# Performance work log

Hardware: AMD Instinct MI355X
Metric: run time of the kernel (lower is better)

Reference implementation:

```python
import jax, jax.numpy as jnp
import numpy as np
import math

# Fixed representative draw of the host-side RNG (all aug probs fired).
MIRROR_X, MIRROR_Y = -1.0, 1.0      # x flip on, y flip off
TX, TY = 0.06, -0.04                # translate percents
SX, SY = 1.1, 0.95                  # anisotropic scale
ZOOM = 0.9                          # isotropic zoom (draws from params['scale'] range in source)
ROT = math.radians(27.0)            # rotate degrees -> rad
SHX, SHY = 0.05, -0.03              # shear percents


def _affine_grid(theta, H, W):
    # torch F.affine_grid with align_corners=False: pixel-center normalized coords
    xs = (jnp.arange(W, dtype=jnp.float32) + 0.5) * (2.0 / W) - 1.0
    ys = (jnp.arange(H, dtype=jnp.float32) + 0.5) * (2.0 / H) - 1.0
    gx, gy = jnp.meshgrid(xs, ys)  # [H,W]
    coords = jnp.stack([gx, gy, jnp.ones_like(gx)], axis=-1)  # [H,W,3]
    return jnp.einsum('ij,hwj->hwi', theta, coords)  # [H,W,2] (x,y); same grid for all batch


def _gather(img, iy, ix, valid):
    # img [B,C,H,W]; iy/ix [H,W] int32; valid [H,W] bool. zeros padding.
    B, C, H, W = img.shape
    idx = (jnp.clip(iy, 0, H - 1) * W + jnp.clip(ix, 0, W - 1)).reshape(-1)
    g = img.reshape(B, C, H * W)[:, :, idx].reshape(B, C, H, W)
    return jnp.where(valid[None, None], g, jnp.zeros((), img.dtype))


def _unnormalize(grid, H, W):
    # align_corners=False unnormalization
    ix = ((grid[..., 0] + 1.0) * W - 1.0) * 0.5
    iy = ((grid[..., 1] + 1.0) * H - 1.0) * 0.5
    return ix, iy


def _grid_sample_bilinear(img, grid):
    B, C, H, W = img.shape
    ix, iy = _unnormalize(grid, H, W)
    x0 = jnp.floor(ix); y0 = jnp.floor(iy)
    wx1 = ix - x0; wx0 = 1.0 - wx1
    wy1 = iy - y0; wy0 = 1.0 - wy1
    x0i = x0.astype(jnp.int32); y0i = y0.astype(jnp.int32)
    x1i = x0i + 1; y1i = y0i + 1
    inb = lambda x, y: (x >= 0) & (x < W) & (y >= 0) & (y < H)
    v00 = _gather(img, y0i, x0i, inb(x0i, y0i))
    v01 = _gather(img, y0i, x1i, inb(x1i, y0i))
    v10 = _gather(img, y1i, x0i, inb(x0i, y1i))
    v11 = _gather(img, y1i, x1i, inb(x1i, y1i))
    out = (v00 * (wy0 * wx0)[None, None] + v01 * (wy0 * wx1)[None, None]
           + v10 * (wy1 * wx0)[None, None] + v11 * (wy1 * wx1)[None, None])
    return out


def _grid_sample_nearest(img, grid):
    B, C, H, W = img.shape
    ix, iy = _unnormalize(grid, H, W)
    xi = jnp.round(ix).astype(jnp.int32)
    yi = jnp.round(iy).astype(jnp.int32)
    valid = (xi >= 0) & (xi < W) & (yi >= 0) & (yi < H)
    return _gather(img, yi, xi, valid)


def _thetas():
    c, s = math.cos(ROT), math.sin(ROT)
    return [
        jnp.array([[MIRROR_X, 0.0, 0.0], [0.0, MIRROR_Y, 0.0]], jnp.float32),  # mirror
        jnp.array([[1.0, 0.0, TX], [0.0, 1.0, TY]], jnp.float32),              # translate
        jnp.array([[SX, 0.0, 0.0], [0.0, SY, 0.0]], jnp.float32),              # scale
        jnp.array([[ZOOM, 0.0, 0.0], [0.0, ZOOM, 0.0]], jnp.float32),          # zoom
        jnp.array([[c, -s, 0.0], [s, c, 0.0]], jnp.float32),                   # rotate
        jnp.array([[1.0, SHX, 0.0], [SHY, 1.0, 0.0]], jnp.float32),            # shear
    ]


def setup_inputs() -> dict:
    key = jax.random.key(0)
    k1, k2 = jax.random.split(key)
    img = jax.random.normal(k1, (16, 3, 512, 512), dtype=jnp.float32)
    label = jax.random.uniform(k2, (16, 3, 512, 512), dtype=jnp.float32)
    return {"img": img, "label": label}


def reference(img, label):
    B, C, H, W = img.shape
    # Sequential resampling, exactly as the torch module: one affine_grid +
    # grid_sample pair per enabled augmentation, bilinear for img / nearest for label.
    for theta in _thetas():
        grid = _affine_grid(theta, H, W)
        img = _grid_sample_bilinear(img, grid)
        label = _grid_sample_nearest(label, grid)
    return img, label
```

## Files before the change

kernel.cpp:

```cpp
#include <hip/hip_runtime.h>
#include <math.h>

#define HW 262144
#define TOTAL 12582912
#define TS 32
#define NT 512
#define P 2
#define NGROUP 24

#define CR 0.8910065241883679f
#define SR 0.45399049973954675f

#define K5CX (255.5f * (1.0f - CR + SR))
#define K5CY (255.5f * (1.0f - SR - CR))

#define W2 52
#define H2 44
#define W3 46
#define H3 45
#define W4 49
#define H4 48
#define W5 36
#define H5 35
#define BUFA_SZ 2352
#define BUFB_SZ 2070

struct Box { int x0, x1, y0, y1; };

__device__ __forceinline__ Box back_box(Box d, float A, float B, float C,
                                        float D, float E, float F) {
    float xa = (float)d.x0, xb = (float)d.x1, ya = (float)d.y0, yb = (float)d.y1;
    float mnx = fminf(A * xa, A * xb) + fminf(B * ya, B * yb) + C;
    float mxx = fmaxf(A * xa, A * xb) + fmaxf(B * ya, B * yb) + C;
    float mny = fminf(D * xa, D * xb) + fminf(E * ya, E * yb) + F;
    float mxy = fmaxf(D * xa, D * xb) + fmaxf(E * ya, E * yb) + F;
    Box s;
    s.x0 = (int)floorf(mnx); s.x1 = (int)floorf(mxx) + 1;
    s.y0 = (int)floorf(mny); s.y1 = (int)floorf(mxy) + 1;
    return s;
}

__device__ __forceinline__ float2 lerp2(float w, float2 a, float2 b) {
    float2 r;
    r.x = fmaf(w, b.x - a.x, a.x);
    r.y = fmaf(w, b.y - a.y, a.y);
    return r;
}

template <bool INT>
__device__ __forceinline__ void s2_eval(int i, const float* __restrict__ gin,
                                        float2* __restrict__ dst, int rx0, int ry0)
{
    int ly = i / W2;
    int lx = i - ly * W2;
    int pxi = rx0 + lx, pyi = ry0 + ly;
    if (INT) {
        int off = ((pyi - 11) << 9) + (496 - pxi);
        float2 o;
        {
            const float* g0 = gin + off;
            float h0 = fmaf(0.36f, g0[-1], 0.64f * g0[0]);
            float h1 = fmaf(0.36f, g0[511], 0.64f * g0[512]);
            o.x = fmaf(0.76f, h1, 0.24f * h0);
        }
        {
            const float* g1 = gin + HW + off;
            float h0 = fmaf(0.36f, g1[-1], 0.64f * g1[0]);
            float h1 = fmaf(0.36f, g1[511], 0.64f * g1[512]);
            o.y = fmaf(0.76f, h1, 0.24f * h0);
        }
        dst[i] = o;
    } else {
        float wx0m = ((unsigned)pxi <= 496u) ? 0.64f : 0.0f;
        float wx1m = ((unsigned)pxi <= 495u) ? 0.36f : 0.0f;
        float wy0m = ((unsigned)(pyi - 11) <= 500u) ? 0.24f : 0.0f;
        float wy1m = ((unsigned)(pyi - 10) <= 501u) ? 0.76f : 0.0f;
        int xc0 = min(max(496 - pxi, 0), 511);
        int xc1 = min(max(495 - pxi, 0), 511);
        int r0 = min(max(pyi - 11, 0), 511) << 9;
        int r1 = min(max(pyi - 10, 0), 511) << 9;
        float2 o;
        #pragma unroll
        for (int p = 0; p < P; ++p) {
            const float* g = gin + p * HW;
            float v00 = g[r0 + xc0], v01 = g[r0 + xc1];
            float v10 = g[r1 + xc0], v11 = g[r1 + xc1];
            float h0 = fmaf(wx1m, v01, wx0m * v00);
            float h1 = fmaf(wx1m, v11, wx0m * v10);
            float val = fmaf(wy1m, h1, wy0m * h0);
            if (p == 0) o.x = val; else o.y = val;
        }
        dst[i] = o;
    }
}

template <int SW, int SH, int DW, bool AXIS, bool INT>
__device__ __forceinline__ void lds_eval(int i, float A, float B, float Cs,
    float D, float E, float Fs, const float2* __restrict__ src,
    float2* __restrict__ dst, int dx0, int dy0)
{
    int ly = i / DW;
    int lx = i - ly * DW;
    int pxi = dx0 + lx, pyi = dy0 + ly;
    float px = (float)pxi, py = (float)pyi;
    float fx = AXIS ? fmaf(A, px, Cs) : fmaf(A, px, fmaf(B, py, Cs));
    float fy = AXIS ? fmaf(E, py, Fs) : fmaf(D, px, fmaf(E, py, Fs));
    float xf = floorf(fx), yf = floorf(fy);
    float wx = fx - xf, wy = fy - yf;
    int x0 = (int)xf, y0 = (int)yf;
    if (!INT) { x0 = min(max(x0, 0), SW - 2); y0 = min(max(y0, 0), SH - 2); }
    const float2* s = src + y0 * SW + x0;
    float2 v00 = s[0], v01 = s[1];
    float2 v10 = s[SW], v11 = s[SW + 1];
    float2 a0 = lerp2(wx, v00, v01);
    float2 a1 = lerp2(wx, v10, v11);
    float2 val = lerp2(wy, a0, a1);
    if (!INT) {
        if ((unsigned)pxi >= 512u || (unsigned)pyi >= 512u) { val.x = 0.f; val.y = 0.f; }
    }
    dst[i] = val;
}

template <int SW, int SH, int DW, int DTOT, bool AXIS, bool INT>
__device__ __forceinline__ void stage_lds(int tid, float A, float B, float Cs,
    float D, float E, float Fs, const float2* __restrict__ src,
    float2* __restrict__ dst, int dx0, int dy0)
{
    constexpr int FULL = DTOT / NT;
    constexpr int TAIL = DTOT - FULL * NT;
    #pragma unroll
    for (int k = 0; k < FULL; ++k)
        lds_eval<SW, SH, DW, AXIS, INT>(tid + k * NT, A, B, Cs, D, E, Fs,
                                        src, dst, dx0, dy0);
    if (TAIL && tid < TAIL)
        lds_eval<SW, SH, DW, AXIS, INT>(tid + FULL * NT, A, B, Cs, D, E, Fs,
                                        src, dst, dx0, dy0);
}

template <bool INT>
__device__ __forceinline__ void s6_eval(int ii, const float2* __restrict__ src,
    float* __restrict__ go, int tx0, int ty0, int sx0, int sy0)
{
    int lx = ii & 31, ly = ii >> 5;
    float px = (float)(tx0 + lx), py = (float)(ty0 + ly);
    float fx = fmaf(0.05f, py, -12.775f - (float)sx0) + px;
    float fy = fmaf(-0.03f, px, 7.665f - (float)sy0) + py;
    float xf = floorf(fx), yf = floorf(fy);
    float wx = fx - xf, wy = fy - yf;
    int x0 = (int)xf, y0 = (int)yf;
    if (!INT) { x0 = min(max(x0, 0), W5 - 2); y0 = min(max(y0, 0), H5 - 2); }
    const float2* s = src + y0 * W5 + x0;
    float2 v00 = s[0], v01 = s[1];
    float2 v10 = s[W5], v11 = s[W5 + 1];
    float2 a0 = lerp2(wx, v00, v01);
    float2 a1 = lerp2(wx, v10, v11);
    float2 val = lerp2(wy, a0, a1);
    int gidx = (ty0 + ly) * 512 + tx0 + lx;
    __builtin_nontemporal_store(val.x, &go[gidx]);
    __builtin_nontemporal_store(val.y, &go[HW + gidx]);
}

template <bool INT>
__device__ __forceinline__ void img_tile(int tid, const float* __restrict__ gin,
    float* __restrict__ go, int tx0, int ty0,
    Box R2, Box R3, Box R4, Box R5, float2* bufA, float2* bufB)
{
    {
        constexpr int FULL = (W2 * H2) / NT;
        constexpr int TAIL = W2 * H2 - FULL * NT;
        #pragma unroll
        for (int k = 0; k < FULL; ++k)
            s2_eval<INT>(tid + k * NT, gin, bufA, R2.x0, R2.y0);
        if (tid < TAIL) s2_eval<INT>(tid + FULL * NT, gin, bufA, R2.x0, R2.y0);
    }
    __syncthreads();
    stage_lds<W2, H2, W3, W3 * H3, true, INT>(tid,
        1.1f, 0.0f, -25.55f - (float)R2.x0,
        0.0f, 0.95f, 12.775f - (float)R2.y0, bufA, bufB, R3.x0, R3.y0);
    __syncthreads();
    stage_lds<W3, H3, W4, W4 * H4, true, INT>(tid,
        0.9f, 0.0f, 25.55f - (float)R3.x0,
        0.0f, 0.9f, 25.55f - (float)R3.y0, bufB, bufA, R4.x0, R4.y0);
    __syncthreads();
    stage_lds<W4, H4, W5, W5 * H5, false, INT>(tid,
        CR, -SR, K5CX - (float)R4.x0,
        SR,  CR, K5CY - (float)R4.y0, bufA, bufB, R5.x0, R5.y0);
    __syncthreads();
    {
        constexpr int FULL = (TS * TS) / NT;
        #pragma unroll
        for (int k = 0; k < FULL; ++k)
            s6_eval<INT>(tid + k * NT, bufB, go, tx0, ty0, R5.x0, R5.y0);
    }
}

__global__ void compose_nearest_map(int* __restrict__ map) {
    int p = blockIdx.x * blockDim.x + threadIdx.x;
    if (p >= HW) return;
    const float TH[6][6] = {
        { 1.0f,  0.05f, 0.0f,  -0.03f, 1.0f,  0.0f },
        { CR,    -SR,   0.0f,   SR,    CR,    0.0f },
        { 0.9f,  0.0f,  0.0f,   0.0f,  0.9f,  0.0f },
        { 1.1f,  0.0f,  0.0f,   0.0f,  0.95f, 0.0f },
        { 1.0f,  0.0f,  0.06f,  0.0f,  1.0f, -0.04f },
        { -1.0f, 0.0f,  0.0f,   0.0f,  1.0f,  0.0f },
    };
    int cx = p & 511, cy = p >> 9;
    bool valid = true;
    #pragma unroll
    for (int s = 0; s < 6; ++s) {
        if (!valid) break;
        float x = (cx + 0.5f) * (2.0f / 512.0f) - 1.0f;
        float y = (cy + 0.5f) * (2.0f / 512.0f) - 1.0f;
        float gx = TH[s][0] * x + TH[s][1] * y + TH[s][2];
        float gy = TH[s][3] * x + TH[s][4] * y + TH[s][5];
        float ix = ((gx + 1.0f) * 512.0f - 1.0f) * 0.5f;
        float iy = ((gy + 1.0f) * 512.0f - 1.0f) * 0.5f;
        float xr = rintf(ix), yr = rintf(iy);
        if (xr < 0.0f || xr > 511.0f || yr < 0.0f || yr > 511.0f) valid = false;
        else { cx = (int)xr; cy = (int)yr; }
    }
    map[p] = valid ? (cy * 512 + cx) : -1;
}

__global__ __launch_bounds__(NT, 8) void fused_all(
    const float* __restrict__ img, const float* __restrict__ lab,
    const int* __restrict__ map, float* __restrict__ oimg,
    float* __restrict__ olab)
{
    __shared__ float2 bufA[BUFA_SZ];
    __shared__ float2 bufB[BUFB_SZ];
    int tid = threadIdx.x;
    int b = blockIdx.x;
    int group = b >> 8, tile = b & 255;
    int tx0 = (tile & 15) * TS, ty0 = (tile >> 4) * TS;
    int pbase = group * P;
    const float* gin = img + pbase * HW;
    const float* lin = lab + pbase * HW;
    float* go = oimg + pbase * HW;
    float* lo = olab + pbase * HW;

    {
        constexpr int FULL = (TS * TS) / NT;
        #pragma unroll
        for (int k = 0; k < FULL; ++k) {
            int ii = tid + k * NT;
            int gidx = (ty0 + (ii >> 5)) * 512 + tx0 + (ii & 31);
            int m = map[gidx];
            float v0 = (m >= 0) ? lin[m] : 0.f;
            float v1 = (m >= 0) ? lin[HW + m] : 0.f;
            __builtin_nontemporal_store(v0, &lo[gidx]);
            __builtin_nontemporal_store(v1, &lo[HW + gidx]);
        }
    }

    Box R6 = {tx0, tx0 + TS - 1, ty0, ty0 + TS - 1};
    Box R5 = back_box(R6, 1.0f, 0.05f, -12.775f, -0.03f, 1.0f, 7.665f);
    R5.x1 = min(R5.x1, R5.x0 + W5 - 1); R5.y1 = min(R5.y1, R5.y0 + H5 - 1);
    Box R4 = back_box(R5, CR, -SR, K5CX, SR, CR, K5CY);
    R4.x1 = min(R4.x1, R4.x0 + W4 - 1); R4.y1 = min(R4.y1, R4.y0 + H4 - 1);
    Box R3 = back_box(R4, 0.9f, 0.0f, 25.55f, 0.0f, 0.9f, 25.55f);
    R3.x1 = min(R3.x1, R3.x0 + W3 - 1); R3.y1 = min(R3.y1, R3.y0 + H3 - 1);
    Box R2 = back_box(R3, 1.1f, 0.0f, -25.55f, 0.0f, 0.95f, 12.775f);

    bool dead = (R2.x1 < 0 || R2.x0 > 511 || R2.y1 < 0 || R2.y0 > 511)
             || (R3.x1 < 0 || R3.x0 > 511 || R3.y1 < 0 || R3.y0 > 511)
             || (R4.x1 < 0 || R4.x0 > 511 || R4.y1 < 0 || R4.y0 > 511)
             || (R5.x1 < 0 || R5.x0 > 511 || R5.y1 < 0 || R5.y0 > 511);
    if (dead) {
        constexpr int FULL = (TS * TS) / NT;
        #pragma unroll
        for (int k = 0; k < FULL; ++k) {
            int ii = tid + k * NT;
            int gidx = (ty0 + (ii >> 5)) * 512 + tx0 + (ii & 31);
            __builtin_nontemporal_store(0.f, &go[gidx]);
            __builtin_nontemporal_store(0.f, &go[HW + gidx]);
        }
        return;
    }

    bool interior =
        R2.x0 >= 0 && R2.x0 + W2 - 1 <= 495 && R2.y0 >= 11 && R2.y0 + H2 - 1 <= 511 &&
        R3.x0 >= 0 && R3.x0 + W3 - 1 <= 511 && R3.y0 >= 0 && R3.y0 + H3 - 1 <= 511 &&
        R4.x0 >= 0 && R4.x0 + W4 - 1 <= 511 && R4.y0 >= 0 && R4.y0 + H4 - 1 <= 511 &&
        R5.x0 >= 0 && R5.x0 + W5 - 1 <= 511 && R5.y0 >= 0 && R5.y0 + H5 - 1 <= 511;

    if (interior)
        img_tile<true >(tid, gin, go, tx0, ty0, R2, R3, R4, R5, bufA, bufB);
    else
        img_tile<false>(tid, gin, go, tx0, ty0, R2, R3, R4, R5, bufA, bufB);
}

extern "C" void kernel_launch(void* const* d_in, const int* in_sizes, int n_in,
                              void* d_out, int out_size, void* d_ws, size_t ws_size,
                              hipStream_t stream) {
    const float* img_in = (const float*)d_in[0];
    const float* lab_in = (const float*)d_in[1];
    float* out_img = (float*)d_out;
    float* out_lab = (float*)d_out + TOTAL;
    int* map = (int*)d_ws;

    compose_nearest_map<<<(HW + 255) / 256, 256, 0, stream>>>(map);
    fused_all<<<NGROUP * 256, NT, 0, stream>>>(img_in, lab_in, map, out_img, out_lab);
}
```

Before: 67.86 us.

## Inline nearest-map composition into fused kernel and pair loads for ILP

Measured after the change: 77.33 us. 14.0% more time.

```diff
diff --git a/kernel.cpp b/kernel.cpp
--- a/kernel.cpp
+++ b/kernel.cpp
@@ -47,57 +47,10 @@
     return r;
 }
 
-template <bool INT>
-__device__ __forceinline__ void s2_eval(int i, const float* __restrict__ gin,
-                                        float2* __restrict__ dst, int rx0, int ry0)
-{
-    int ly = i / W2;
-    int lx = i - ly * W2;
-    int pxi = rx0 + lx, pyi = ry0 + ly;
-    if (INT) {
-        int off = ((pyi - 11) << 9) + (496 - pxi);
-        float2 o;
-        {
-            const float* g0 = gin + off;
-            float h0 = fmaf(0.36f, g0[-1], 0.64f * g0[0]);
-            float h1 = fmaf(0.36f, g0[511], 0.64f * g0[512]);
-            o.x = fmaf(0.76f, h1, 0.24f * h0);
-        }
-        {
-            const float* g1 = gin + HW + off;
-            float h0 = fmaf(0.36f, g1[-1], 0.64f * g1[0]);
-            float h1 = fmaf(0.36f, g1[511], 0.64f * g1[512]);
-            o.y = fmaf(0.76f, h1, 0.24f * h0);
-        }
-        dst[i] = o;
-    } else {
-        float wx0m = ((unsigned)pxi <= 496u) ? 0.64f : 0.0f;
-        float wx1m = ((unsigned)pxi <= 495u) ? 0.36f : 0.0f;
-        float wy0m = ((unsigned)(pyi - 11) <= 500u) ? 0.24f : 0.0f;
-        float wy1m = ((unsigned)(pyi - 10) <= 501u) ? 0.76f : 0.0f;
-        int xc0 = min(max(496 - pxi, 0), 511);
-        int xc1 = min(max(495 - pxi, 0), 511);
-        int r0 = min(max(pyi - 11, 0), 511) << 9;
-        int r1 = min(max(pyi - 10, 0), 511) << 9;
-        float2 o;
-        #pragma unroll
-        for (int p = 0; p < P; ++p) {
-            const float* g = gin + p * HW;
-            float v00 = g[r0 + xc0], v01 = g[r0 + xc1];
-            float v10 = g[r1 + xc0], v11 = g[r1 + xc1];
-            float h0 = fmaf(wx1m, v01, wx0m * v00);
-            float h1 = fmaf(wx1m, v11, wx0m * v10);
-            float val = fmaf(wy1m, h1, wy0m * h0);
-            if (p == 0) o.x = val; else o.y = val;
-        }
-        dst[i] = o;
-    }
-}
-
 template <int SW, int SH, int DW, bool AXIS, bool INT>
-__device__ __forceinline__ void lds_eval(int i, float A, float B, float Cs,
-    float D, float E, float Fs, const float2* __restrict__ src,
-    float2* __restrict__ dst, int dx0, int dy0)
+__device__ __forceinline__ void lds_geom(int i, float A, float B, float Cs,
+    float D, float E, float Fs, int dx0, int dy0,
+    int& sbase, float& wx, float& wy, bool& oob)
 {
     int ly = i / DW;
     int lx = i - ly * DW;
@@ -106,19 +59,11 @@
     float fx = AXIS ? fmaf(A, px, Cs) : fmaf(A, px, fmaf(B, py, Cs));
     float fy = AXIS ? fmaf(E, py, Fs) : fmaf(D, px, fmaf(E, py, Fs));
     float xf = floorf(fx), yf = floorf(fy);
-    float wx = fx - xf, wy = fy - yf;
+    wx = fx - xf; wy = fy - yf;
     int x0 = (int)xf, y0 = (int)yf;
     if (!INT) { x0 = min(max(x0, 0), SW - 2); y0 = min(max(y0, 0), SH - 2); }
-    const float2* s = src + y0 * SW + x0;
-    float2 v00 = s[0], v01 = s[1];
-    float2 v10 = s[SW], v11 = s[SW + 1];
-    float2 a0 = lerp2(wx, v00, v01);
-    float2 a1 = lerp2(wx, v10, v11);
-    float2 val = lerp2(wy, a0, a1);
-    if (!INT) {
-        if ((unsigned)pxi >= 512u || (unsigned)pyi >= 512u) { val.x = 0.f; val.y = 0.f; }
-    }
-    dst[i] = val;
+    sbase = y0 * SW + x0;
+    oob = (!INT) && ((unsigned)pxi >= 512u || (unsigned)pyi >= 512u);
 }
 
 template <int SW, int SH, int DW, int DTOT, bool AXIS, bool INT>
@@ -126,38 +71,185 @@
     float D, float E, float Fs, const float2* __restrict__ src,
     float2* __restrict__ dst, int dx0, int dy0)
 {
-    constexpr int FULL = DTOT / NT;
-    constexpr int TAIL = DTOT - FULL * NT;
+    constexpr int NITEM = (DTOT + NT - 1) / NT;
     #pragma unroll
-    for (int k = 0; k < FULL; ++k)
-        lds_eval<SW, SH, DW, AXIS, INT>(tid + k * NT, A, B, Cs, D, E, Fs,
-                                        src, dst, dx0, dy0);
-    if (TAIL && tid < TAIL)
-        lds_eval<SW, SH, DW, AXIS, INT>(tid + FULL * NT, A, B, Cs, D, E, Fs,
-                                        src, dst, dx0, dy0);
+    for (int k = 0; k < NITEM; k += 2) {
+        constexpr int KMAX = NITEM;
+        const bool HAS1 = (k + 1 < KMAX);
+        int i0 = tid + k * NT;
+        int i1 = i0 + NT;
+        bool w0 = (i0 < DTOT);
+        bool w1 = HAS1 && (i1 < DTOT);
+        int c0 = min(i0, DTOT - 1);
+        int c1 = min(i1, DTOT - 1);
+
+        int s0, s1 = 0; float wx0, wy0, wx1 = 0.f, wy1 = 0.f; bool o0, o1 = false;
+        lds_geom<SW, SH, DW, AXIS, INT>(c0, A, B, Cs, D, E, Fs, dx0, dy0,
+                                        s0, wx0, wy0, o0);
+        if (HAS1)
+            lds_geom<SW, SH, DW, AXIS, INT>(c1, A, B, Cs, D, E, Fs, dx0, dy0,
+                                            s1, wx1, wy1, o1);
+
+        float2 q00 = src[s0], q01 = src[s0 + 1];
+        float2 q10 = src[s0 + SW], q11 = src[s0 + SW + 1];
+        float2 r00, r01, r10, r11;
+        if (HAS1) { r00 = src[s1]; r01 = src[s1 + 1];
+                    r10 = src[s1 + SW]; r11 = src[s1 + SW + 1]; }
+
+        {
+            float2 a0 = lerp2(wx0, q00, q01);
+            float2 a1 = lerp2(wx0, q10, q11);
+            float2 val = lerp2(wy0, a0, a1);
+            if (!INT && o0) { val.x = 0.f; val.y = 0.f; }
+            if (w0) dst[c0] = val;
+        }
+        if (HAS1) {
+            float2 a0 = lerp2(wx1, r00, r01);
+            float2 a1 = lerp2(wx1, r10, r11);
+            float2 val = lerp2(wy1, a0, a1);
+            if (!INT && o1) { val.x = 0.f; val.y = 0.f; }
+            if (w1) dst[c1] = val;
+        }
+    }
 }
 
 template <bool INT>
-__device__ __forceinline__ void s6_eval(int ii, const float2* __restrict__ src,
+__device__ __forceinline__ void s2_geom(int i, int rx0, int ry0,
+    int& off0, int& off1, float& wx0m, float& wx1m, float& wy0m, float& wy1m)
+{
+    int ly = i / W2;
+    int lx = i - ly * W2;
+    int pxi = rx0 + lx, pyi = ry0 + ly;
+    if (INT) {
+        off0 = ((pyi - 11) << 9) + (496 - pxi);
+        off1 = off0;
+        wx0m = 0.64f; wx1m = 0.36f; wy0m = 0.24f; wy1m = 0.76f;
+    } else {
+        wx0m = ((unsigned)pxi <= 496u) ? 0.64f : 0.0f;
+        wx1m = ((unsigned)pxi <= 495u) ? 0.36f : 0.0f;
+        wy0m = ((unsigned)(pyi - 11) <= 500u) ? 0.24f : 0.0f;
+        wy1m = ((unsigned)(pyi - 10) <= 501u) ? 0.76f : 0.0f;
+        int xc0 = min(max(496 - pxi, 0), 511);
+        int r0 = min(max(pyi - 11, 0), 511) << 9;
+        int r1 = min(max(pyi - 10, 0), 511) << 9;
+        off0 = r0 + xc0;
+        off1 = r1 + xc0;
+    }
+}
+
+template <bool INT>
+__device__ __forceinline__ void s2_pair(int tid, int k, const float* __restrict__ gin,
+                                        float2* __restrict__ dst, int rx0, int ry0,
+                                        bool has1)
+{
+    int i0 = tid + k * NT;
+    int i1 = i0 + NT;
+    bool w0 = (i0 < W2 * H2);
+    bool w1 = has1 && (i1 < W2 * H2);
+    int c0 = min(i0, W2 * H2 - 1);
+    int c1 = min(i1, W2 * H2 - 1);
+
+    if (INT) {
+        int ly0 = c0 / W2, lx0 = c0 - ly0 * W2;
+        int ly1 = c1 / W2, lx1 = c1 - ly1 * W2;
+        int offA = ((ry0 + ly0 - 11) << 9) + (496 - (rx0 + lx0));
+        int offB = ((ry0 + ly1 - 11) << 9) + (496 - (rx0 + lx1));
+        const float* gA0 = gin + offA;
+        const float* gA1 = gin + HW + offA;
+        const float* gB0 = gin + offB;
+        const float* gB1 = gin + HW + offB;
+        float a00 = gA0[0], a01 = gA0[-1], a02 = gA0[512], a03 = gA0[511];
+        float a10 = gA1[0], a11 = gA1[-1], a12 = gA1[512], a13 = gA1[511];
+        float b00 = 0.f, b01 = 0.f, b02 = 0.f, b03 = 0.f;
+        float b10 = 0.f, b11 = 0.f, b12 = 0.f, b13 = 0.f;
+        if (has1) {
+            b00 = gB0[0]; b01 = gB0[-1]; b02 = gB0[512]; b03 = gB0[511];
+            b10 = gB1[0]; b11 = gB1[-1]; b12 = gB1[512]; b13 = gB1[511];
+        }
+        float2 o0, o1;
+        o0.x = fmaf(0.76f, fmaf(0.36f, a03, 0.64f * a02),
+                    0.24f * fmaf(0.36f, a01, 0.64f * a00));
+        o0.y = fmaf(0.76f, fmaf(0.36f, a13, 0.64f * a12),
+                    0.24f * fmaf(0.36f, a11, 0.64f * a10));
+        if (w0) dst[c0] = o0;
+        if (has1) {
+            o1.x = fmaf(0.76f, fmaf(0.36f, b03, 0.64f * b02),
+                        0.24f * fmaf(0.36f, b01, 0.64f * b00));
+            o1.y = fmaf(0.76f, fmaf(0.36f, b13, 0.64f * b12),
+                        0.24f * fmaf(0.36f, b11, 0.64f * b10));
+            if (w1) dst[c1] = o1;
+        }
+    } else {
+        #pragma unroll
+        for (int t = 0; t < 2; ++t) {
+            if (t == 1 && !has1) break;
+            int c = (t == 0) ? c0 : c1;
+            bool w = (t == 0) ? w0 : w1;
+            int ly = c / W2, lx = c - ly * W2;
+            int pxi = rx0 + lx, pyi = ry0 + ly;
+            float wx0m = ((unsigned)pxi <= 496u) ? 0.64f : 0.0f;
+            float wx1m = ((unsigned)pxi <= 495u) ? 0.36f : 0.0f;
+            float wy0m = ((unsigned)(pyi - 11) <= 500u) ? 0.24f : 0.0f;
+            float wy1m = ((unsigned)(pyi - 10) <= 501u) ? 0.76f : 0.0f;
+            int xc0 = min(max(496 - pxi, 0), 511);
+            int xc1 = min(max(495 - pxi, 0), 511);
+            int r0 = min(max(pyi - 11, 0), 511) << 9;
+            int r1 = min(max(pyi - 10, 0), 511) << 9;
+            float2 o;
+            #pragma unroll
+            for (int p = 0; p < P; ++p) {
+                const float* g = gin + p * HW;
+                float v00 = g[r0 + xc0], v01 = g[r0 + xc1];
+                float v10 = g[r1 + xc0], v11 = g[r1 + xc1];
+                float h0 = fmaf(wx1m, v01, wx0m * v00);
+                float h1 = fmaf(wx1m, v11, wx0m * v10);
+                float val = fmaf(wy1m, h1, wy0m * h0);
+                if (p == 0) o.x = val; else o.y = val;
+            }
+            if (w) dst[c] = o;
+        }
+    }
+}
+
+template <bool INT>
+__device__ __forceinline__ void s6_both(int tid, const float2* __restrict__ src,
     float* __restrict__ go, int tx0, int ty0, int sx0, int sy0)
 {
-    int lx = ii & 31, ly = ii >> 5;
-    float px = (float)(tx0 + lx), py = (float)(ty0 + ly);
-    float fx = fmaf(0.05f, py, -12.775f - (float)sx0) + px;
-    float fy = fmaf(-0.03f, px, 7.665f - (float)sy0) + py;
-    float xf = floorf(fx), yf = floorf(fy);
-    float wx = fx - xf, wy = fy - yf;
-    int x0 = (int)xf, y0 = (int)yf;
-    if (!INT) { x0 = min(max(x0, 0), W5 - 2); y0 = min(max(y0, 0), H5 - 2); }
-    const float2* s = src + y0 * W5 + x0;
-    float2 v00 = s[0], v01 = s[1];
-    float2 v10 = s[W5], v11 = s[W5 + 1];
-    float2 a0 = lerp2(wx, v00, v01);
-    float2 a1 = lerp2(wx, v10, v11);
-    float2 val = lerp2(wy, a0, a1);
-    int gidx = (ty0 + ly) * 512 + tx0 + lx;
-    __builtin_nontemporal_store(val.x, &go[gidx]);
-    __builtin_nontemporal_store(val.y, &go[HW + gidx]);
+    float Csx = -12.775f - (float)sx0;
+    float Fsy = 7.665f - (float)sy0;
+    int s[2]; float wx[2], wy[2]; int gidx[2];
+    #pragma unroll
+    for (int t = 0; t < 2; ++t) {
+        int ii = tid + t * NT;
+        int lx = ii & 31, ly = ii >> 5;
+        float px = (float)(tx0 + lx), py = (float)(ty0 + ly);
+        float fx = fmaf(0.05f, py, Csx) + px;
+        float fy = fmaf(-0.03f, px, Fsy) + py;
+        float xf = floorf(fx), yf = floorf(fy);
+        wx[t] = fx - xf; wy[t] = fy - yf;
+        int x0 = (int)xf, y0 = (int)yf;
+        if (!INT) { x0 = min(max(x0, 0), W5 - 2); y0 = min(max(y0, 0), H5 - 2); }
+        s[t] = y0 * W5 + x0;
+        gidx[t] = (ty0 + ly) * 512 + tx0 + lx;
+    }
+    float2 q00 = src[s[0]], q01 = src[s[0] + 1];
+    float2 q10 = src[s[0] + W5], q11 = src[s[0] + W5 + 1];
+    float2 r00 = src[s[1]], r01 = src[s[1] + 1];
+    float2 r10 = src[s[1] + W5], r11 = src[s[1] + W5 + 1];
+    {
+        float2 a0 = lerp2(wx[0], q00, q01);
+        float2 a1 = lerp2(wx[0], q10, q11);
+        float2 val = lerp2(wy[0], a0, a1);
+        __builtin_nontemporal_store(val.x, &go[gidx[0]]);
+        __builtin_nontemporal_store(val.y, &go[HW + gidx[0]]);
+    }
+    {
+        float2 a0 = lerp2(wx[1], r00, r01);
+        float2 a1 = lerp2(wx[1], r10, r11);
+        float2 val = lerp2(wy[1], a0, a1);
+        __builtin_nontemporal_store(val.x, &go[gidx[1]]);
+        __builtin_nontemporal_store(val.y, &go[HW + gidx[1]]);
+    }
 }
 
 template <bool INT>
@@ -165,14 +257,9 @@
     float* __restrict__ go, int tx0, int ty0,
     Box R2, Box R3, Box R4, Box R5, float2* bufA, float2* bufB)
 {
-    {
-        constexpr int FULL = (W2 * H2) / NT;
-        constexpr int TAIL = W2 * H2 - FULL * NT;
-        #pragma unroll
-        for (int k = 0; k < FULL; ++k)
-            s2_eval<INT>(tid + k * NT, gin, bufA, R2.x0, R2.y0);
-        if (tid < TAIL) s2_eval<INT>(tid + FULL * NT, gin, bufA, R2.x0, R2.y0);
-    }
+    s2_pair<INT>(tid, 0, gin, bufA, R2.x0, R2.y0, true);
+    s2_pair<INT>(tid, 2, gin, bufA, R2.x0, R2.y0, true);
+    s2_pair<INT>(tid, 4, gin, bufA, R2.x0, R2.y0, false);
     __syncthreads();
     stage_lds<W2, H2, W3, W3 * H3, true, INT>(tid,
         1.1f, 0.0f, -25.55f - (float)R2.x0,
@@ -186,47 +273,12 @@
         CR, -SR, K5CX - (float)R4.x0,
         SR,  CR, K5CY - (float)R4.y0, bufA, bufB, R5.x0, R5.y0);
     __syncthreads();
-    {
-        constexpr int FULL = (TS * TS) / NT;
-        #pragma unroll
-        for (int k = 0; k < FULL; ++k)
-            s6_eval<INT>(tid + k * NT, bufB, go, tx0, ty0, R5.x0, R5.y0);
-    }
-}
-
-__global__ void compose_nearest_map(int* __restrict__ map) {
-    int p = blockIdx.x * blockDim.x + threadIdx.x;
-    if (p >= HW) return;
-    const float TH[6][6] = {
-        { 1.0f,  0.05f, 0.0f,  -0.03f, 1.0f,  0.0f },
-        { CR,    -SR,   0.0f,   SR,    CR,    0.0f },
-        { 0.9f,  0.0f,  0.0f,   0.0f,  0.9f,  0.0f },
-        { 1.1f,  0.0f,  0.0f,   0.0f,  0.95f, 0.0f },
-        { 1.0f,  0.0f,  0.06f,  0.0f,  1.0f, -0.04f },
-        { -1.0f, 0.0f,  0.0f,   0.0f,  1.0f,  0.0f },
-    };
-    int cx = p & 511, cy = p >> 9;
-    bool valid = true;
-    #pragma unroll
-    for (int s = 0; s < 6; ++s) {
-        if (!valid) break;
-        float x = (cx + 0.5f) * (2.0f / 512.0f) - 1.0f;
-        float y = (cy + 0.5f) * (2.0f / 512.0f) - 1.0f;
-        float gx = TH[s][0] * x + TH[s][1] * y + TH[s][2];
-        float gy = TH[s][3] * x + TH[s][4] * y + TH[s][5];
-        float ix = ((gx + 1.0f) * 512.0f - 1.0f) * 0.5f;
-        float iy = ((gy + 1.0f) * 512.0f - 1.0f) * 0.5f;
-        float xr = rintf(ix), yr = rintf(iy);
-        if (xr < 0.0f || xr > 511.0f || yr < 0.0f || yr > 511.0f) valid = false;
-        else { cx = (int)xr; cy = (int)yr; }
-    }
-    map[p] = valid ? (cy * 512 + cx) : -1;
+    s6_both<INT>(tid, bufB, go, tx0, ty0, R5.x0, R5.y0);
 }
 
 __global__ __launch_bounds__(NT, 8) void fused_all(
     const float* __restrict__ img, const float* __restrict__ lab,
-    const int* __restrict__ map, float* __restrict__ oimg,
-    float* __restrict__ olab)
+    float* __restrict__ oimg, float* __restrict__ olab)
 {
     __shared__ float2 bufA[BUFA_SZ];
     __shared__ float2 bufB[BUFB_SZ];
@@ -241,17 +293,47 @@
     float* lo = olab + pbase * HW;
 
     {
-        constexpr int FULL = (TS * TS) / NT;
+        const float TH[6][6] = {
+            { 1.0f,  0.05f, 0.0f,  -0.03f, 1.0f,  0.0f },
+            { CR,    -SR,   0.0f,   SR,    CR,    0.0f },
+            { 0.9f,  0.0f,  0.0f,   0.0f,  0.9f,  0.0f },
+            { 1.1f,  0.0f,  0.0f,   0.0f,  0.95f, 0.0f },
+            { 1.0f,  0.0f,  0.06f,  0.0f,  1.0f, -0.04f },
+            { -1.0f, 0.0f,  0.0f,   0.0f,  1.0f,  0.0f },
+        };
+        int m[2]; bool valid[2]; int gidx[2];
         #pragma unroll
-        for (int k = 0; k < FULL; ++k) {
-            int ii = tid + k * NT;
-            int gidx = (ty0 + (ii >> 5)) * 512 + tx0 + (ii & 31);
-            int m = map[gidx];
-            float v0 = (m >= 0) ? lin[m] : 0.f;
-            float v1 = (m >= 0) ? lin[HW + m] : 0.f;
-            __builtin_nontemporal_store(v0, &lo[gidx]);
-            __builtin_nontemporal_store(v1, &lo[HW + gidx]);
-        }
+        for (int t = 0; t < 2; ++t) {
+            int ii = tid + t * NT;
+            int lx = ii & 31, ly = ii >> 5;
+            int cx = tx0 + lx, cy = ty0 + ly;
+            gidx[t] = cy * 512 + cx;
+            bool v = true;
+            #pragma unroll
+            for (int s = 0; s < 6; ++s) {
+                float x = ((float)cx + 0.5f) * (2.0f / 512.0f) - 1.0f;
+                float y = ((float)cy + 0.5f) * (2.0f / 512.0f) - 1.0f;
+                float gx = TH[s][0] * x + TH[s][1] * y + TH[s][2];
+                float gy = TH[s][3] * x + TH[s][4] * y + TH[s][5];
+                float ix = ((gx + 1.0f) * 512.0f - 1.0f) * 0.5f;
+                float iy = ((gy + 1.0f) * 512.0f - 1.0f) * 0.5f;
+                float xr = rintf(ix), yr = rintf(iy);
+                bool ok = (xr >= 0.0f && xr <= 511.0f && yr >= 0.0f && yr <= 511.0f);
+                v = v && ok;
+                cx = (int)fminf(fmaxf(xr, 0.0f), 511.0f);
+                cy = (int)fminf(fmaxf(yr, 0.0f), 511.0f);
+            }
+            valid[t] = v;
+            m[t] = cy * 512 + cx;
+        }
+        float v00 = valid[0] ? lin[m[0]] : 0.f;
+        float v01 = valid[0] ? lin[HW + m[0]] : 0.f;
+        float v10 = valid[1] ? lin[m[1]] : 0.f;
+        float v11 = valid[1] ? lin[HW + m[1]] : 0.f;
+        __builtin_nontemporal_store(v00, &lo[gidx[0]]);
+        __builtin_nontemporal_store(v01, &lo[HW + gidx[0]]);
+        __builtin_nontemporal_store(v10, &lo[gidx[1]]);
+        __builtin_nontemporal_store(v11, &lo[HW + gidx[1]]);
     }
 
     Box R6 = {tx0, tx0 + TS - 1, ty0, ty0 + TS - 1};
@@ -268,9 +350,8 @@
              || (R4.x1 < 0 || R4.x0 > 511 || R4.y1 < 0 || R4.y0 > 511)
              || (R5.x1 < 0 || R5.x0 > 511 || R5.y1 < 0 || R5.y0 > 511);
     if (dead) {
-        constexpr int FULL = (TS * TS) / NT;
         #pragma unroll
-        for (int k = 0; k < FULL; ++k) {
+        for (int k = 0; k < (TS * TS) / NT; ++k) {
             int ii = tid + k * NT;
             int gidx = (ty0 + (ii >> 5)) * 512 + tx0 + (ii & 31);
             __builtin_nontemporal_store(0.f, &go[gidx]);
@@ -298,8 +379,7 @@
     const float* lab_in = (const float*)d_in[1];
     float* out_img = (float*)d_out;
     float* out_lab = (float*)d_out + TOTAL;
-    int* map = (int*)d_ws;
-
-    compose_nearest_map<<<(HW + 255) / 256, 256, 0, stream>>>(map);
-    fused_all<<<NGROUP * 256, NT, 0, stream>>>(img_in, lab_in, map, out_img, out_lab);
-}
+    (void)d_ws; (void)ws_size;
+
+    fused_all<<<NGROUP * 256, NT, 0, stream>>>(img_in, lab_in, out_img, out_lab);
+}
```

## Fuse bilinear stage pairs into 3x3 composite taps on interior tiles

Applied to the files above, without the earlier changes.

New measurement: 75.77 us. 11.6% more time.

```diff
diff --git a/kernel.cpp b/kernel.cpp
--- a/kernel.cpp
+++ b/kernel.cpp
@@ -47,55 +47,134 @@
     return r;
 }
 
-template <bool INT>
-__device__ __forceinline__ void s2_eval(int i, const float* __restrict__ gin,
-                                        float2* __restrict__ dst, int rx0, int ry0)
+
+__device__ __forceinline__ void s23_eval(int i, const float* __restrict__ gin,
+                                         float2* __restrict__ dst, int r3x0, int r3y0)
+{
+    int ly = i / W3;
+    int lx = i - ly * W3;
+    float px = (float)(r3x0 + lx), py = (float)(r3y0 + ly);
+    float fx = fmaf(1.1f, px, -25.55f);
+    float fy = fmaf(0.95f, py, 12.775f);
+    float xf = floorf(fx), yf = floorf(fy);
+    float wx = fx - xf, wy = fy - yf;
+    int x0 = (int)xf, y0 = (int)yf;
+    int off = ((y0 - 11) << 9) + (496 - x0);
+    const float* g0 = gin + off;
+    const float* g1 = g0 + HW;
+    float u0 = fmaf(-0.64f, wx, 0.64f);
+    float u1 = fmaf(0.28f, wx, 0.36f);
+    float u2 = 0.36f * wx;
+    float t0 = fmaf(-0.24f, wy, 0.24f);
+    float t1 = fmaf(-0.52f, wy, 0.76f);
+    float t2 = 0.76f * wy;
+    float a0 = g0[0],    a1 = g0[-1],   a2 = g0[-2];
+    float a3 = g0[512],  a4 = g0[511],  a5 = g0[510];
+    float a6 = g0[1024], a7 = g0[1023], a8 = g0[1022];
+    float b0 = g1[0],    b1 = g1[-1],   b2 = g1[-2];
+    float b3 = g1[512],  b4 = g1[511],  b5 = g1[510];
+    float b6 = g1[1024], b7 = g1[1023], b8 = g1[1022];
+    float r0a = fmaf(u0, a0, fmaf(u1, a1, u2 * a2));
+    float r1a = fmaf(u0, a3, fmaf(u1, a4, u2 * a5));
+    float r2a = fmaf(u0, a6, fmaf(u1, a7, u2 * a8));
+    float r0b = fmaf(u0, b0, fmaf(u1, b1, u2 * b2));
+    float r1b = fmaf(u0, b3, fmaf(u1, b4, u2 * b5));
+    float r2b = fmaf(u0, b6, fmaf(u1, b7, u2 * b8));
+    float2 o;
+    o.x = fmaf(t0, r0a, fmaf(t1, r1a, t2 * r2a));
+    o.y = fmaf(t0, r0b, fmaf(t1, r1b, t2 * r2b));
+    dst[i] = o;
+}
+
+__device__ __forceinline__ void s45_eval(int i, const float2* __restrict__ src,
+                                         float2* __restrict__ dst,
+                                         int r5x0, int r5y0, int r3x0, int r3y0)
+{
+    int ly = i / W5;
+    int lx = i - ly * W5;
+    float px = (float)(r5x0 + lx), py = (float)(r5y0 + ly);
+    float fx5 = fmaf(CR, px, fmaf(-SR, py, K5CX));
+    float fy5 = fmaf(SR, px, fmaf(CR, py, K5CY));
+    float x5f = floorf(fx5), y5f = floorf(fy5);
+    float wx5 = fx5 - x5f, wy5 = fy5 - y5f;
+
+    float fx40 = fmaf(0.9f, x5f, 25.55f);
+    float bxf = floorf(fx40);  float w40 = fx40 - bxf;
+    float fx41 = fx40 + 0.9f;
+    float bx1f = floorf(fx41); float w41 = fx41 - bx1f;
+    float mx = (bx1f == bxf) ? 1.0f : 0.0f;
+    float iwx5 = 1.0f - wx5;
+    float ax0 = iwx5 * (1.0f - w40), ax1 = iwx5 * w40;
+    float bx0 = wx5 * (1.0f - w41),  bx1w = wx5 * w41;
+    float cw0 = fmaf(mx, bx0, ax0);
+    float cw1 = ax1 + fmaf(mx, bx1w, (1.0f - mx) * bx0);
+    float cw2 = (1.0f - mx) * bx1w;
+
+    float fy40 = fmaf(0.9f, y5f, 25.55f);
+    float byf = floorf(fy40);  float v40 = fy40 - byf;
+    float fy41 = fy40 + 0.9f;
+    float by1f = floorf(fy41); float v41 = fy41 - by1f;
+    float my = (by1f == byf) ? 1.0f : 0.0f;
+    float iwy5 = 1.0f - wy5;
+    float ay0 = iwy5 * (1.0f - v40), ay1 = iwy5 * v40;
+    float by0 = wy5 * (1.0f - v41),  by1w = wy5 * v41;
+    float rw0 = fmaf(my, by0, ay0);
+    float rw1 = ay1 + fmaf(my, by1w, (1.0f - my) * by0);
+    float rw2 = (1.0f - my) * by1w;
+
+    int cb = min(max((int)bxf - r3x0, 0), W3 - 2);
+    int rb = min(max((int)byf - r3y0, 0), H3 - 2);
+    int c2 = min(cb + 2, W3 - 1);
+    int r2 = min(rb + 2, H3 - 1);
+    const float2* s0 = src + rb * W3;
+    const float2* s1 = s0 + W3;
+    const float2* s2 = src + r2 * W3;
+    float2 A0 = s0[cb], A1 = s0[cb + 1], A2 = s0[c2];
+    float2 B0 = s1[cb], B1 = s1[cb + 1], B2 = s1[c2];
+    float2 C0 = s2[cb], C1 = s2[cb + 1], C2 = s2[c2];
+    float rAx = fmaf(cw0, A0.x, fmaf(cw1, A1.x, cw2 * A2.x));
+    float rAy = fmaf(cw0, A0.y, fmaf(cw1, A1.y, cw2 * A2.y));
+    float rBx = fmaf(cw0, B0.x, fmaf(cw1, B1.x, cw2 * B2.x));
+    float rBy = fmaf(cw0, B0.y, fmaf(cw1, B1.y, cw2 * B2.y));
+    float rCx = fmaf(cw0, C0.x, fmaf(cw1, C1.x, cw2 * C2.x));
+    float rCy = fmaf(cw0, C0.y, fmaf(cw1, C1.y, cw2 * C2.y));
+    float2 o;
+    o.x = fmaf(rw0, rAx, fmaf(rw1, rBx, rw2 * rCx));
+    o.y = fmaf(rw0, rAy, fmaf(rw1, rBy, rw2 * rCy));
+    dst[i] = o;
+}
+
+
+__device__ __forceinline__ void s2_eval_gen(int i, const float* __restrict__ gin,
+                                            float2* __restrict__ dst, int rx0, int ry0)
 {
     int ly = i / W2;
     int lx = i - ly * W2;
     int pxi = rx0 + lx, pyi = ry0 + ly;
-    if (INT) {
-        int off = ((pyi - 11) << 9) + (496 - pxi);
-        float2 o;
-        {
-            const float* g0 = gin + off;
-            float h0 = fmaf(0.36f, g0[-1], 0.64f * g0[0]);
-            float h1 = fmaf(0.36f, g0[511], 0.64f * g0[512]);
-            o.x = fmaf(0.76f, h1, 0.24f * h0);
-        }
-        {
-            const float* g1 = gin + HW + off;
-            float h0 = fmaf(0.36f, g1[-1], 0.64f * g1[0]);
-            float h1 = fmaf(0.36f, g1[511], 0.64f * g1[512]);
-            o.y = fmaf(0.76f, h1, 0.24f * h0);
-        }
-        dst[i] = o;
-    } else {
-        float wx0m = ((unsigned)pxi <= 496u) ? 0.64f : 0.0f;
-        float wx1m = ((unsigned)pxi <= 495u) ? 0.36f : 0.0f;
-        float wy0m = ((unsigned)(pyi - 11) <= 500u) ? 0.24f : 0.0f;
-        float wy1m = ((unsigned)(pyi - 10) <= 501u) ? 0.76f : 0.0f;
-        int xc0 = min(max(496 - pxi, 0), 511);
-        int xc1 = min(max(495 - pxi, 0), 511);
-        int r0 = min(max(pyi - 11, 0), 511) << 9;
-        int r1 = min(max(pyi - 10, 0), 511) << 9;
-        float2 o;
-        #pragma unroll
-        for (int p = 0; p < P; ++p) {
-            const float* g = gin + p * HW;
-            float v00 = g[r0 + xc0], v01 = g[r0 + xc1];
-            float v10 = g[r1 + xc0], v11 = g[r1 + xc1];
-            float h0 = fmaf(wx1m, v01, wx0m * v00);
-            float h1 = fmaf(wx1m, v11, wx0m * v10);
-            float val = fmaf(wy1m, h1, wy0m * h0);
-            if (p == 0) o.x = val; else o.y = val;
-        }
-        dst[i] = o;
-    }
-}
-
-template <int SW, int SH, int DW, bool AXIS, bool INT>
-__device__ __forceinline__ void lds_eval(int i, float A, float B, float Cs,
+    float wx0m = ((unsigned)pxi <= 496u) ? 0.64f : 0.0f;
+    float wx1m = ((unsigned)pxi <= 495u) ? 0.36f : 0.0f;
+    float wy0m = ((unsigned)(pyi - 11) <= 500u) ? 0.24f : 0.0f;
+    float wy1m = ((unsigned)(pyi - 10) <= 501u) ? 0.76f : 0.0f;
+    int xc0 = min(max(496 - pxi, 0), 511);
+    int xc1 = min(max(495 - pxi, 0), 511);
+    int r0 = min(max(pyi - 11, 0), 511) << 9;
+    int r1 = min(max(pyi - 10, 0), 511) << 9;
+    float2 o;
+    #pragma unroll
+    for (int p = 0; p < P; ++p) {
+        const float* g = gin + p * HW;
+        float v00 = g[r0 + xc0], v01 = g[r0 + xc1];
+        float v10 = g[r1 + xc0], v11 = g[r1 + xc1];
+        float h0 = fmaf(wx1m, v01, wx0m * v00);
+        float h1 = fmaf(wx1m, v11, wx0m * v10);
+        float val = fmaf(wy1m, h1, wy0m * h0);
+        if (p == 0) o.x = val; else o.y = val;
+    }
+    dst[i] = o;
+}
+
+template <int SW, int SH, int DW, bool AXIS>
+__device__ __forceinline__ void lds_eval_gen(int i, float A, float B, float Cs,
     float D, float E, float Fs, const float2* __restrict__ src,
     float2* __restrict__ dst, int dx0, int dy0)
 {
@@ -107,22 +186,20 @@
     float fy = AXIS ? fmaf(E, py, Fs) : fmaf(D, px, fmaf(E, py, Fs));
     float xf = floorf(fx), yf = floorf(fy);
     float wx = fx - xf, wy = fy - yf;
-    int x0 = (int)xf, y0 = (int)yf;
-    if (!INT) { x0 = min(max(x0, 0), SW - 2); y0 = min(max(y0, 0), SH - 2); }
+    int x0 = min(max((int)xf, 0), SW - 2);
+    int y0 = min(max((int)yf, 0), SH - 2);
     const float2* s = src + y0 * SW + x0;
     float2 v00 = s[0], v01 = s[1];
     float2 v10 = s[SW], v11 = s[SW + 1];
     float2 a0 = lerp2(wx, v00, v01);
     float2 a1 = lerp2(wx, v10, v11);
     float2 val = lerp2(wy, a0, a1);
-    if (!INT) {
-        if ((unsigned)pxi >= 512u || (unsigned)pyi >= 512u) { val.x = 0.f; val.y = 0.f; }
-    }
+    if ((unsigned)pxi >= 512u || (unsigned)pyi >= 512u) { val.x = 0.f; val.y = 0.f; }
     dst[i] = val;
 }
 
-template <int SW, int SH, int DW, int DTOT, bool AXIS, bool INT>
-__device__ __forceinline__ void stage_lds(int tid, float A, float B, float Cs,
+template <int SW, int SH, int DW, int DTOT, bool AXIS>
+__device__ __forceinline__ void stage_lds_gen(int tid, float A, float B, float Cs,
     float D, float E, float Fs, const float2* __restrict__ src,
     float2* __restrict__ dst, int dx0, int dy0)
 {
@@ -130,11 +207,11 @@
     constexpr int TAIL = DTOT - FULL * NT;
     #pragma unroll
     for (int k = 0; k < FULL; ++k)
-        lds_eval<SW, SH, DW, AXIS, INT>(tid + k * NT, A, B, Cs, D, E, Fs,
-                                        src, dst, dx0, dy0);
+        lds_eval_gen<SW, SH, DW, AXIS>(tid + k * NT, A, B, Cs, D, E, Fs,
+                                       src, dst, dx0, dy0);
     if (TAIL && tid < TAIL)
-        lds_eval<SW, SH, DW, AXIS, INT>(tid + FULL * NT, A, B, Cs, D, E, Fs,
-                                        src, dst, dx0, dy0);
+        lds_eval_gen<SW, SH, DW, AXIS>(tid + FULL * NT, A, B, Cs, D, E, Fs,
+                                       src, dst, dx0, dy0);
 }
 
 template <bool INT>
@@ -160,8 +237,34 @@
     __builtin_nontemporal_store(val.y, &go[HW + gidx]);
 }
 
-template <bool INT>
-__device__ __forceinline__ void img_tile(int tid, const float* __restrict__ gin,
+__device__ __forceinline__ void img_tile_fast(int tid, const float* __restrict__ gin,
+    float* __restrict__ go, int tx0, int ty0, Box R3, Box R5,
+    float2* bufA, float2* bufB)
+{
+    {
+        constexpr int FULL = (W3 * H3) / NT;
+        constexpr int TAIL = W3 * H3 - FULL * NT;
+        #pragma unroll
+        for (int k = 0; k < FULL; ++k)
+            s23_eval(tid + k * NT, gin, bufB, R3.x0, R3.y0);
+        if (tid < TAIL) s23_eval(tid + FULL * NT, gin, bufB, R3.x0, R3.y0);
+    }
+    __syncthreads();
+    {
+        constexpr int FULL = (W5 * H5) / NT;
+        constexpr int TAIL = W5 * H5 - FULL * NT;
+        #pragma unroll
+        for (int k = 0; k < FULL; ++k)
+            s45_eval(tid + k * NT, bufB, bufA, R5.x0, R5.y0, R3.x0, R3.y0);
+        if (tid < TAIL) s45_eval(tid + FULL * NT, bufB, bufA, R5.x0, R5.y0, R3.x0, R3.y0);
+    }
+    __syncthreads();
+    #pragma unroll
+    for (int k = 0; k < (TS * TS) / NT; ++k)
+        s6_eval<true>(tid + k * NT, bufA, go, tx0, ty0, R5.x0, R5.y0);
+}
+
+__device__ __forceinline__ void img_tile_gen(int tid, const float* __restrict__ gin,
     float* __restrict__ go, int tx0, int ty0,
     Box R2, Box R3, Box R4, Box R5, float2* bufA, float2* bufB)
 {
@@ -170,28 +273,25 @@
         constexpr int TAIL = W2 * H2 - FULL * NT;
         #pragma unroll
         for (int k = 0; k < FULL; ++k)
-            s2_eval<INT>(tid + k * NT, gin, bufA, R2.x0, R2.y0);
-        if (tid < TAIL) s2_eval<INT>(tid + FULL * NT, gin, bufA, R2.x0, R2.y0);
-    }
-    __syncthreads();
-    stage_lds<W2, H2, W3, W3 * H3, true, INT>(tid,
+            s2_eval_gen(tid + k * NT, gin, bufA, R2.x0, R2.y0);
+        if (tid < TAIL) s2_eval_gen(tid + FULL * NT, gin, bufA, R2.x0, R2.y0);
+    }
+    __syncthreads();
+    stage_lds_gen<W2, H2, W3, W3 * H3, true>(tid,
         1.1f, 0.0f, -25.55f - (float)R2.x0,
         0.0f, 0.95f, 12.775f - (float)R2.y0, bufA, bufB, R3.x0, R3.y0);
     __syncthreads();
-    stage_lds<W3, H3, W4, W4 * H4, true, INT>(tid,
+    stage_lds_gen<W3, H3, W4, W4 * H4, true>(tid,
         0.9f, 0.0f, 25.55f - (float)R3.x0,
         0.0f, 0.9f, 25.55f - (float)R3.y0, bufB, bufA, R4.x0, R4.y0);
     __syncthreads();
-    stage_lds<W4, H4, W5, W5 * H5, false, INT>(tid,
+    stage_lds_gen<W4, H4, W5, W5 * H5, false>(tid,
         CR, -SR, K5CX - (float)R4.x0,
         SR,  CR, K5CY - (float)R4.y0, bufA, bufB, R5.x0, R5.y0);
     __syncthreads();
-    {
-        constexpr int FULL = (TS * TS) / NT;
-        #pragma unroll
-        for (int k = 0; k < FULL; ++k)
-            s6_eval<INT>(tid + k * NT, bufB, go, tx0, ty0, R5.x0, R5.y0);
-    }
+    #pragma unroll
+    for (int k = 0; k < (TS * TS) / NT; ++k)
+        s6_eval<false>(tid + k * NT, bufB, go, tx0, ty0, R5.x0, R5.y0);
 }
 
 __global__ void compose_nearest_map(int* __restrict__ map) {
@@ -240,18 +340,15 @@
     float* go = oimg + pbase * HW;
     float* lo = olab + pbase * HW;
 
-    {
-        constexpr int FULL = (TS * TS) / NT;
-        #pragma unroll
-        for (int k = 0; k < FULL; ++k) {
-            int ii = tid + k * NT;
-            int gidx = (ty0 + (ii >> 5)) * 512 + tx0 + (ii & 31);
-            int m = map[gidx];
-            float v0 = (m >= 0) ? lin[m] : 0.f;
-            float v1 = (m >= 0) ? lin[HW + m] : 0.f;
-            __builtin_nontemporal_store(v0, &lo[gidx]);
-            __builtin_nontemporal_store(v1, &lo[HW + gidx]);
-        }
+    #pragma unroll
+    for (int k = 0; k < (TS * TS) / NT; ++k) {
+        int ii = tid + k * NT;
+        int gidx = (ty0 + (ii >> 5)) * 512 + tx0 + (ii & 31);
+        int m = map[gidx];
+        float v0 = (m >= 0) ? lin[m] : 0.f;
+        float v1 = (m >= 0) ? lin[HW + m] : 0.f;
+        __builtin_nontemporal_store(v0, &lo[gidx]);
+        __builtin_nontemporal_store(v1, &lo[HW + gidx]);
     }
 
     Box R6 = {tx0, tx0 + TS - 1, ty0, ty0 + TS - 1};
@@ -268,9 +365,8 @@
              || (R4.x1 < 0 || R4.x0 > 511 || R4.y1 < 0 || R4.y0 > 511)
              || (R5.x1 < 0 || R5.x0 > 511 || R5.y1 < 0 || R5.y0 > 511);
     if (dead) {
-        constexpr int FULL = (TS * TS) / NT;
         #pragma unroll
-        for (int k = 0; k < FULL; ++k) {
+        for (int k = 0; k < (TS * TS) / NT; ++k) {
             int ii = tid + k * NT;
             int gidx = (ty0 + (ii >> 5)) * 512 + tx0 + (ii & 31);
             __builtin_nontemporal_store(0.f, &go[gidx]);
@@ -286,9 +382,9 @@
         R5.x0 >= 0 && R5.x0 + W5 - 1 <= 511 && R5.y0 >= 0 && R5.y0 + H5 - 1 <= 511;
 
     if (interior)
-        img_tile<true >(tid, gin, go, tx0, ty0, R2, R3, R4, R5, bufA, bufB);
+        img_tile_fast(tid, gin, go, tx0, ty0, R3, R5, bufA, bufB);
     else
-        img_tile<false>(tid, gin, go, tx0, ty0, R2, R3, R4, R5, bufA, bufB);
+        img_tile_gen(tid, gin, go, tx0, ty0, R2, R3, R4, R5, bufA, bufB);
 }
 
 extern "C" void kernel_launch(void* const* d_in, const int* in_sizes, int n_in,
```
